# Performance work log

Measured on AMD Instinct MI355X. Metric: run time of the kernel, lower is better.

## Reference

```python
import jax, jax.numpy as jnp
import numpy as np

B, T, D, H = 64, 1024, 1, 256  # batch, seq_len, input_size(=output_size), hidden_size


def setup_inputs() -> dict:
    key = jax.random.key(0)
    ks = jax.random.split(key, 16)
    s = 1.0 / np.sqrt(H)  # torch LSTM/Linear default uniform init scale
    u = lambda k, shp: jax.random.uniform(k, shp, jnp.float32, -s, s)
    return {
        "x": jax.random.normal(ks[0], (B, T, D), jnp.float32),
        # encoder bidirectional 2-layer LSTM; leading dim 2 = (fwd, bwd); gate order i,f,g,o
        "enc_Wih_l0": u(ks[1], (2, 4 * H, D)),
        "enc_Whh_l0": u(ks[2], (2, 4 * H, H)),
        "enc_b_l0": u(ks[3], (2, 4 * H)),
        "enc_Wih_l1": u(ks[4], (2, 4 * H, 2 * H)),
        "enc_Whh_l1": u(ks[5], (2, 4 * H, H)),
        "enc_b_l1": u(ks[6], (2, 4 * H)),
        # decoder bidirectional 2-layer LSTM
        "dec_Wih_l0": u(ks[7], (2, 4 * H, D)),
        "dec_Whh_l0": u(ks[8], (2, 4 * H, H)),
        "dec_b_l0": u(ks[9], (2, 4 * H)),
        "dec_Wih_l1": u(ks[10], (2, 4 * H, 2 * H)),
        "dec_Whh_l1": u(ks[11], (2, 4 * H, H)),
        "dec_b_l1": u(ks[12], (2, 4 * H)),
        # output projection: Linear(2H -> 1)
        "fc_W": u(ks[13], (1, 2 * H)),
        "fc_b": u(ks[14], (1,)),
    }


def _cell(xt, h, c, Wih, Whh, b):
    # one LSTM cell step; xt: (B, Din), h/c: (B, H)
    gates = xt @ Wih.T + h @ Whh.T + b
    i, f, g, o = jnp.split(gates, 4, axis=-1)  # torch gate order i,f,g,o
    c = jax.nn.sigmoid(f) * c + jax.nn.sigmoid(i) * jnp.tanh(g)
    h = jax.nn.sigmoid(o) * jnp.tanh(c)
    return h, c


def _scan_dir(xs, Wih, Whh, b, reverse):
    # xs: (T, B, Din) time-major; returns (T,B,H) outputs aligned to input order + final (h,c)
    bsz = xs.shape[1]
    h0 = jnp.zeros((bsz, H), xs.dtype)
    def step(carry, xt):
        h, c = _cell(xt, carry[0], carry[1], Wih, Whh, b)
        return (h, c), h
    (hT, cT), ys = jax.lax.scan(step, (h0, h0), xs, reverse=reverse)
    return ys, hT, cT


def reference(x, enc_Wih_l0, enc_Whh_l0, enc_b_l0, enc_Wih_l1, enc_Whh_l1, enc_b_l1,
              dec_Wih_l0, dec_Whh_l0, dec_b_l0, dec_Wih_l1, dec_Whh_l1, dec_b_l1,
              fc_W, fc_b):
    xT = jnp.transpose(x, (1, 0, 2))  # (T, B, D)
    # ---- encoder: 2-layer bidirectional LSTM, zero initial state ----
    yf0, hf0, cf0 = _scan_dir(xT, enc_Wih_l0[0], enc_Whh_l0[0], enc_b_l0[0], False)
    yb0, hb0, cb0 = _scan_dir(xT, enc_Wih_l0[1], enc_Whh_l0[1], enc_b_l0[1], True)
    y0 = jnp.concatenate([yf0, yb0], axis=-1)  # (T, B, 2H)
    _, hf1, cf1 = _scan_dir(y0, enc_Wih_l1[0], enc_Whh_l1[0], enc_b_l1[0], False)
    _, hb1, cb1 = _scan_dir(y0, enc_Wih_l1[1], enc_Whh_l1[1], enc_b_l1[1], True)
    # torch state layout: [l0_fwd, l0_bwd, l1_fwd, l1_bwd]
    eh = (hf0, hb0, hf1, hb1)
    ec = (cf0, cb0, cf1, cb1)

    # ---- decoder: each step re-initializes LSTM state from ENCODER state (source bug,
    # reproduced faithfully); only the fc output feeds back as the next input ----
    def dec_step(x_in, _):
        hf, _c1 = _cell(x_in, eh[0], ec[0], dec_Wih_l0[0], dec_Whh_l0[0], dec_b_l0[0])
        hb, _c2 = _cell(x_in, eh[1], ec[1], dec_Wih_l0[1], dec_Whh_l0[1], dec_b_l0[1])
        z = jnp.concatenate([hf, hb], axis=-1)  # (B, 2H)
        hf1_, _c3 = _cell(z, eh[2], ec[2], dec_Wih_l1[0], dec_Whh_l1[0], dec_b_l1[0])
        hb1_, _c4 = _cell(z, eh[3], ec[3], dec_Wih_l1[1], dec_Whh_l1[1], dec_b_l1[1])
        y = jnp.concatenate([hf1_, hb1_], axis=-1) @ fc_W.T + fc_b  # (B, 1)
        return y, y

    x0 = jnp.zeros((x.shape[0], x.shape[2]), x.dtype)
    _, ys = jax.lax.scan(dec_step, x0, None, length=x.shape[1])  # (T, B, 1)
    return jnp.transpose(ys, (1, 0, 2))  # (B, T, 1)
```

## Files before the change

kernel.cpp:

```cpp
#include <hip/hip_runtime.h>
#include <hip/hip_bf16.h>
#include <hip/hip_fp16.h>
#include <math.h>


#define NWG 256
#define THR 512
#define U0S 132

#define ECL0   2048
#define EHL1   (ECL0 + 32768)
#define ECL1   (EHL1 + 16384)
#define ROF    (ECL1 + 32768)
#define WIH1T  (ROF + 262144)
#define GWR    (WIH1T + 524288)
#define PCF    (GWR + 1048576)
#define Y0OF   (PCF + 8192)
#define WS_REQ_BYTES ((size_t)(Y0OF + 16777216) * 4)

struct SeqParams {
  const void *x, *eWih0, *eWhh0, *eB0, *eWih1, *eWhh1, *eB1;
  const void *dWih0, *dWhh0, *dB0, *dWih1, *dWhh1, *dB1, *fcW, *fcb;
  void* out;
  float* ws;
  unsigned* ctrs;
};

typedef _Float16 hlf2 __attribute__((ext_vector_type(2)));

__device__ __forceinline__ float bf2f(unsigned short u) {
  return __uint_as_float(((unsigned)u) << 16);
}
__device__ __forceinline__ float hf2f(unsigned short u) {
  __half_raw r; r.x = u; return __half2float(__half(r));
}
__device__ __forceinline__ unsigned short f2h_u(float f) {
  __half h = __float2half(f);
  return *reinterpret_cast<unsigned short*>(&h);
}

__device__ __forceinline__ float fexp2(float x) {
#if __has_builtin(__builtin_amdgcn_exp2f)
  return __builtin_amdgcn_exp2f(x);
#else
  return exp2f(x);
#endif
}
__device__ __forceinline__ float frcp(float x) {
#if __has_builtin(__builtin_amdgcn_rcpf)
  return __builtin_amdgcn_rcpf(x);
#else
  return 1.0f / x;
#endif
}
__device__ __forceinline__ float sigm(float v) {
  return frcp(1.0f + fexp2(v * -1.44269504f));
}
__device__ __forceinline__ float ftanh(float v) {
  return fmaf(-2.0f, frcp(1.0f + fexp2(v * 2.88539008f)), 1.0f);
}

#if __has_builtin(__builtin_amdgcn_fdot2)
__device__ __forceinline__ float fdot2(hlf2 a, hlf2 b, float c) {
  return __builtin_amdgcn_fdot2(a, b, c, false);
}
#else
__device__ __forceinline__ float fdot2(hlf2 a, hlf2 b, float c) {
  return c + (float)a[0] * (float)b[0] + (float)a[1] * (float)b[1];
}
#endif

__device__ __forceinline__ float dot1(float a, const uint4& x, const uint4& y) {
  const hlf2* xp = reinterpret_cast<const hlf2*>(&x);
  const hlf2* yp = reinterpret_cast<const hlf2*>(&y);
  a = fdot2(xp[0], yp[0], a);
  a = fdot2(xp[1], yp[1], a);
  a = fdot2(xp[2], yp[2], a);
  a = fdot2(xp[3], yp[3], a);
  return a;
}
__device__ __forceinline__ void dot2acc(float4& a, const uint4& hv, const uint4& wv) {
  const hlf2* hp = reinterpret_cast<const hlf2*>(&hv);
  const hlf2* wp = reinterpret_cast<const hlf2*>(&wv);
  a.x = fdot2(hp[0], wp[0], a.x);
  a.y = fdot2(hp[1], wp[1], a.y);
  a.z = fdot2(hp[2], wp[2], a.z);
  a.w = fdot2(hp[3], wp[3], a.w);
}

__device__ __forceinline__ float ldin(const void* p_, size_t i, int bf) {
  return bf ? bf2f(((const unsigned short*)p_)[i]) : ((const float*)p_)[i];
}
__device__ __forceinline__ void stout(void* o, size_t i, float v, int bf) {
  if (bf) ((__hip_bfloat16*)o)[i] = __float2bfloat16(v);
  else    ((float*)o)[i] = v;
}

__device__ __forceinline__ int detect_bf16(const void* xp) {
  const unsigned* u = (const unsigned*)xp;
  int votes = 0;
#pragma unroll 8
  for (int i = 0; i < 64; ++i) {
    unsigned e = (u[i] >> 7) & 0xFF;
    votes += (e >= 108 && e <= 131) ? 1 : 0;
  }
  return votes >= 32;
}

__device__ __forceinline__ void gbar(unsigned* ctrs, unsigned gen) {
  __syncthreads();
  if (threadIdx.x == 0) {
    __hip_atomic_fetch_add(&ctrs[(blockIdx.x & 31) * 32], 1u,
                           __ATOMIC_RELEASE, __HIP_MEMORY_SCOPE_AGENT);
  }
  if (threadIdx.x < 32) {
    while (__hip_atomic_load(&ctrs[threadIdx.x * 32], __ATOMIC_RELAXED,
                             __HIP_MEMORY_SCOPE_AGENT) < gen * 8u) {
      __builtin_amdgcn_s_sleep(1);
    }
    (void)__hip_atomic_load(&ctrs[threadIdx.x * 32], __ATOMIC_ACQUIRE,
                            __HIP_MEMORY_SCOPE_AGENT);
  }
  __syncthreads();
}

__device__ __forceinline__ uint4 ldw8(const void* src, size_t off, int bf) {
  union { __half h[8]; uint4 u; } r;
  if (bf) {
    const unsigned short* s = (const unsigned short*)src + off;
    ushort4 a = *reinterpret_cast<const ushort4*>(s);
    ushort4 b = *reinterpret_cast<const ushort4*>(s + 4);
    r.h[0] = __float2half(bf2f(a.x)); r.h[1] = __float2half(bf2f(a.y));
    r.h[2] = __float2half(bf2f(a.z)); r.h[3] = __float2half(bf2f(a.w));
    r.h[4] = __float2half(bf2f(b.x)); r.h[5] = __float2half(bf2f(b.y));
    r.h[6] = __float2half(bf2f(b.z)); r.h[7] = __float2half(bf2f(b.w));
  } else {
    const float* s = (const float*)src + off;
    float4 a = *reinterpret_cast<const float4*>(s);
    float4 b = *reinterpret_cast<const float4*>(s + 4);
    r.h[0] = __float2half(a.x); r.h[1] = __float2half(a.y);
    r.h[2] = __float2half(a.z); r.h[3] = __float2half(a.w);
    r.h[4] = __float2half(b.x); r.h[5] = __float2half(b.y);
    r.h[6] = __float2half(b.z); r.h[7] = __float2half(b.w);
  }
  return r.u;
}

__device__ __forceinline__ void stage_u128(unsigned* AH, const unsigned* src,
                                           int ustr, int uoff) {
  const int t = threadIdx.x;
#pragma unroll
  for (int i = 0; i < 4; ++i) {
    int idx = t + i * THR;
    int r = idx >> 5, c4 = (idx & 31) << 2;
    uint4 v = *reinterpret_cast<const uint4*>(src + (size_t)r * ustr + uoff + c4);
    *reinterpret_cast<uint4*>(AH + r * U0S + c4) = v;
  }
}
__device__ __forceinline__ void load_w16_rows(uint4 (&wr)[2][4], const void* src,
                                              int rowbase, int bf) {
  const int t = threadIdx.x, kc = t >> 6, rt = t & 3;
#pragma unroll
  for (int j = 0; j < 2; ++j) {
    size_t rb = (size_t)(rowbase + rt * 2 + j) * 256 + kc * 32;
#pragma unroll
    for (int d = 0; d < 4; ++d) wr[j][d] = ldw8(src, rb + d * 8, bf);
  }
}
__device__ __forceinline__ void dot2_t4(float4* acc, const unsigned* A,
                                        const uint4 (&wr)[2][4]) {
  const int t = threadIdx.x;
  const int kc = t >> 6, bt = (t & 63) >> 2;
#pragma unroll
  for (int d = 0; d < 4; ++d) {
    const int k = kc * 16 + d * 4;
    uint4 h0 = *reinterpret_cast<const uint4*>(A + (bt +  0) * U0S + k);
    uint4 h1 = *reinterpret_cast<const uint4*>(A + (bt + 16) * U0S + k);
    uint4 h2 = *reinterpret_cast<const uint4*>(A + (bt + 32) * U0S + k);
    uint4 h3 = *reinterpret_cast<const uint4*>(A + (bt + 48) * U0S + k);
    dot2acc(acc[0], h0, wr[0][d]); dot2acc(acc[1], h0, wr[1][d]);
    dot2acc(acc[2], h1, wr[0][d]); dot2acc(acc[3], h1, wr[1][d]);
    dot2acc(acc[4], h2, wr[0][d]); dot2acc(acc[5], h2, wr[1][d]);
    dot2acc(acc[6], h3, wr[0][d]); dot2acc(acc[7], h3, wr[1][d]);
  }
}
__device__ __forceinline__ void reduce_R(const float4* acc, float* part, float* dst,
                                         const void* bsrc, int rowbase, int bf) {
  const int t = threadIdx.x;
  const int kc = t >> 6, tile = t & 63;
#pragma unroll
  for (int e = 0; e < 8; ++e) {
    const float4 a = acc[e];
    part[e * 512 + kc * 64 + tile] = (a.x + a.y) + (a.z + a.w);
  }
  __syncthreads();
  {
    const int r = t >> 6, b = t & 63;
    const int tl = (b & 15) * 4 + (r >> 1);
    const float* pp = part + ((b >> 4) * 2 + (r & 1)) * 512 + tl;
    float v = ((pp[0] + pp[64]) + (pp[128] + pp[192])) +
              ((pp[256] + pp[320]) + (pp[384] + pp[448]));
    dst[(size_t)b * 1024 + rowbase + r] = v + ldin(bsrc, rowbase + r, bf);
  }
  __syncthreads();
}

__global__ void __launch_bounds__(THR, 2)
__attribute__((amdgpu_waves_per_eu(2, 2)))
seq2seq_kernel(SeqParams p) {
  __shared__ __align__(16) char smem[148224];
  uint4* WLDSu4 = (uint4*)smem;
  float* GF     = (float*)(smem + 131072);
  float* PREB   = (float*)(smem + 135168);
  float* PREWf  = (float*)(smem + 139264);
  float* XROW   = (float*)(smem + 143360);
  unsigned* H16 = (unsigned*)(smem + 147456);
  float* YL     = (float*)(smem + 147968);

  const int w = blockIdx.x;
  const int t = threadIdx.x;
  float* ws = p.ws;
  unsigned* ctrs = p.ctrs;
  unsigned* y0w   = (unsigned*)(ws + Y0OF);
  unsigned* EHL1u = (unsigned*)(ws + EHL1);
  uint4* WIH1Tu4  = (uint4*)(ws + WIH1T);
  unsigned* GWu   = (unsigned*)(ws + GWR);
  unsigned* flg   = (unsigned*)(ws + PCF);
  uint4* DWu4     = (uint4*)(ws + Y0OF);
  unsigned genF = 0;
  const int bfm = detect_bf16(p.x);
  const int enc_act = (w < 128);
  const int d = (w >> 6) & 1, b = w & 63;
  const int R0 = t >> 1, hs = t & 1, swz = R0 & 7;

  uint4 wreg3[3][16];

  {
    if (w == 0) {
      for (int i = t; i < 8192; i += THR) flg[i] = 0u;
    }
    if (enc_act) {
      const void* whh0 = bfm ? (const void*)((const unsigned short*)p.eWhh0 + (size_t)d * 262144)
                             : (const void*)((const float*)p.eWhh0 + (size_t)d * 262144);
#pragma unroll
      for (int sl = 0; sl < 3; ++sl)
#pragma unroll
        for (int kk = 0; kk < 16; ++kk)
          wreg3[sl][kk] = ldw8(whh0, (size_t)(R0 + sl * 256) * 256 + (size_t)hs * 128 + kk * 8, bfm);
#pragma unroll
      for (int i = 0; i < 16; ++i) {
        int idx = t + i * 512;
        int row = idx >> 5, j = idx & 31;
        WLDSu4[row * 32 + (j ^ (row & 7))] =
            ldw8(whh0, (size_t)(768 + row) * 256 + j * 8, bfm);
      }
#pragma unroll
      for (int q = 0; q < 2; ++q) {
        PREB[t + q * 512]  = ldin(p.eB0,   d * 1024 + t + q * 512, bfm);
        PREWf[t + q * 512] = ldin(p.eWih0, d * 1024 + t + q * 512, bfm);
        XROW[t + q * 512]  = ldin(p.x, (size_t)b * 1024 + t + q * 512, bfm);
      }
      if (t < 128) H16[t] = 0u;
    }
  }
  gbar(ctrs, ++genF);

  if (enc_act) {
    float cc = 0.f;
    const uint4* wl = WLDSu4 + R0 * 32;
    for (int st = 0; st < 1024; ++st) {
      const int tt = d ? (1023 - st) : st;
      float s0 = 0.f, s1 = 0.f, s2 = 0.f, s3 = 0.f;
#pragma unroll
      for (int hb = 0; hb < 2; ++hb) {
        uint4 wlv[8], hvv[8];
#pragma unroll
        for (int i = 0; i < 8; ++i) {
          int ii = hb * 8 + i;
          wlv[i] = wl[(hs * 16 + ii) ^ swz];
          hvv[i] = *(const uint4*)(H16 + hs * 64 + ii * 4);
        }
#pragma unroll
        for (int i = 0; i < 8; ++i) {
          int ii = hb * 8 + i;
          s0 = dot1(s0, hvv[i], wreg3[0][ii]);
          s1 = dot1(s1, hvv[i], wreg3[1][ii]);
          s2 = dot1(s2, hvv[i], wreg3[2][ii]);
          s3 = dot1(s3, hvv[i], wlv[i]);
        }
      }
      s0 += __shfl_xor(s0, 1, 64);
      s1 += __shfl_xor(s1, 1, 64);
      s2 += __shfl_xor(s2, 1, 64);
      s3 += __shfl_xor(s3, 1, 64);
      if (hs == 0) { GF[R0] = s0;       GF[R0 + 256] = s1; }
      else         { GF[R0 + 512] = s2; GF[768 + R0] = s3; }
      __syncthreads();
      if (t < 256) {
        float xv = XROW[tt];
        float gi = GF[t]       + PREB[t]       + xv * PREWf[t];
        float gf = GF[256 + t] + PREB[256 + t] + xv * PREWf[256 + t];
        float gg = GF[512 + t] + PREB[512 + t] + xv * PREWf[512 + t];
        float go = GF[768 + t] + PREB[768 + t] + xv * PREWf[768 + t];
        float cn = sigm(gf) * cc + sigm(gi) * ftanh(gg);
        float hn = sigm(go) * ftanh(cn);
        cc = cn;
        ((unsigned short*)H16)[t] = f2h_u(hn);
        if (st == 1023) ws[ECL0 + d * 16384 + b * 256 + t] = cn;
      }
      __syncthreads();
      if (t < 128) y0w[(size_t)tt * 16384 + (size_t)b * 256 + d * 128 + t] = H16[t];
    }
  }
  gbar(ctrs, ++genF);

  {
    {
      int idx = w * 512 + t;
      int dd = idx >> 16, rem = idx & 65535;
      int kc = rem >> 10, row = rem & 1023;
      WIH1Tu4[idx] = ldw8(p.eWih1, (size_t)dd * 524288 + (size_t)row * 512 + kc * 8, bfm);
    }
    if (enc_act) {
      const void* whh1 = bfm ? (const void*)((const unsigned short*)p.eWhh1 + (size_t)d * 262144)
                             : (const void*)((const float*)p.eWhh1 + (size_t)d * 262144);
#pragma unroll
      for (int sl = 0; sl < 3; ++sl)
#pragma unroll
        for (int kk = 0; kk < 16; ++kk)
          wreg3[sl][kk] = ldw8(whh1, (size_t)(R0 + sl * 256) * 256 + (size_t)hs * 128 + kk * 8, bfm);
#pragma unroll
      for (int i = 0; i < 16; ++i) {
        int idx = t + i * 512;
        int row = idx >> 5, j = idx & 31;
        WLDSu4[row * 32 + (j ^ (row & 7))] =
            ldw8(whh1, (size_t)(768 + row) * 256 + j * 8, bfm);
      }
#pragma unroll
      for (int q = 0; q < 2; ++q)
        PREB[t + q * 512] = ldin(p.eB1, d * 1024 + t + q * 512, bfm);
      if (t < 128) H16[t] = 0u;
    }
  }
  gbar(ctrs, ++genF);

  if (enc_act) {
    float cc = 0.f;
    const uint4* wl = WLDSu4 + R0 * 32;
    for (int st = 0; st < 1024; ++st) {
      const int win = st >> 3, sl = st & 7;
      if (sl == 0) {
        if (t == 0) {
          while (__hip_atomic_load(&flg[w * 64], __ATOMIC_RELAXED,
                                   __HIP_MEMORY_SCOPE_AGENT) < (unsigned)(win + 1)) {
            __builtin_amdgcn_s_sleep(1);
          }
        }
        __atomic_signal_fence(__ATOMIC_ACQUIRE);
        __syncthreads();
      }
      unsigned g0 = 0, g1 = 0;
      if (t < 256) {
        const unsigned gb = (unsigned)w * 8192 + (unsigned)(win & 1) * 4096 + (unsigned)sl * 512;
        g0 = __hip_atomic_load(&GWu[gb + t],       __ATOMIC_RELAXED, __HIP_MEMORY_SCOPE_AGENT);
        g1 = __hip_atomic_load(&GWu[gb + 256 + t], __ATOMIC_RELAXED, __HIP_MEMORY_SCOPE_AGENT);
      }
      float s0 = 0.f, s1 = 0.f, s2 = 0.f, s3 = 0.f;
#pragma unroll
      for (int hb = 0; hb < 2; ++hb) {
        uint4 wlv[8], hvv[8];
#pragma unroll
        for (int i = 0; i < 8; ++i) {
          int ii = hb * 8 + i;
          wlv[i] = wl[(hs * 16 + ii) ^ swz];
          hvv[i] = *(const uint4*)(H16 + hs * 64 + ii * 4);
        }
#pragma unroll
        for (int i = 0; i < 8; ++i) {
          int ii = hb * 8 + i;
          s0 = dot1(s0, hvv[i], wreg3[0][ii]);
          s1 = dot1(s1, hvv[i], wreg3[1][ii]);
          s2 = dot1(s2, hvv[i], wreg3[2][ii]);
          s3 = dot1(s3, hvv[i], wlv[i]);
        }
      }
      s0 += __shfl_xor(s0, 1, 64);
      s1 += __shfl_xor(s1, 1, 64);
      s2 += __shfl_xor(s2, 1, 64);
      s3 += __shfl_xor(s3, 1, 64);
      if (hs == 0) { GF[R0] = s0;       GF[R0 + 256] = s1; }
      else         { GF[R0 + 512] = s2; GF[768 + R0] = s3; }
      __syncthreads();
      if (t < 256) {
        float gi = GF[t]       + PREB[t]       + hf2f((unsigned short)(g0 & 0xffffu));
        float gf = GF[256 + t] + PREB[256 + t] + hf2f((unsigned short)(g1 & 0xffffu));
        float gg = GF[512 + t] + PREB[512 + t] + hf2f((unsigned short)(g0 >> 16));
        float go = GF[768 + t] + PREB[768 + t] + hf2f((unsigned short)(g1 >> 16));
        float cn = sigm(gf) * cc + sigm(gi) * ftanh(gg);
        float hn = sigm(go) * ftanh(cn);
        cc = cn;
        ((unsigned short*)H16)[t] = f2h_u(hn);
        if (st == 1023) ws[ECL1 + d * 16384 + b * 256 + t] = cn;
      }
      __syncthreads();
      if (st == 1023 && t < 128) EHL1u[d * 8192 + b * 128 + t] = H16[t];
      if (sl == 7 && t == 0)
        __hip_atomic_store(&flg[w * 64 + 32], (unsigned)(win + 1),
                           __ATOMIC_RELAXED, __HIP_MEMORY_SCOPE_AGENT);
    }
  } else {
    const int chain = w - 128, dp = chain >> 6, bp = chain & 63;
    const uint4* Wt = WIH1Tu4 + (size_t)dp * 65536;
    uint4* YWu4 = (uint4*)smem;
    for (int win = 0; win < 128; ++win) {
      if (win >= 2) {
        if (t == 0) {
          while (__hip_atomic_load(&flg[chain * 64 + 32], __ATOMIC_RELAXED,
                                   __HIP_MEMORY_SCOPE_AGENT) < (unsigned)(win - 1)) {
            __builtin_amdgcn_s_sleep(1);
          }
        }
        __syncthreads();
      }
      {
        int s = t >> 6, kcc = t & 63;
        int tw = dp ? (1023 - (win * 8 + s)) : (win * 8 + s);
        YWu4[s * 64 + kcc] =
            *(const uint4*)(y0w + (size_t)tw * 16384 + (size_t)bp * 256 + kcc * 4);
      }
      __syncthreads();
      float a0[8], a1[8];
#pragma unroll
      for (int s = 0; s < 8; ++s) { a0[s] = 0.f; a1[s] = 0.f; }
      for (int kc = 0; kc < 64; ++kc) {
        uint4 w0 = Wt[kc * 1024 + t];
        uint4 w1 = Wt[kc * 1024 + 512 + t];
#pragma unroll
        for (int s = 0; s < 8; ++s) {
          uint4 yv = YWu4[s * 64 + kc];
          a0[s] = dot1(a0[s], yv, w0);
          a1[s] = dot1(a1[s], yv, w1);
        }
      }
      const unsigned gb = (unsigned)chain * 8192 + (unsigned)(win & 1) * 4096;
#pragma unroll
      for (int s = 0; s < 8; ++s) {
        unsigned pw = (unsigned)f2h_u(a0[s]) | ((unsigned)f2h_u(a1[s]) << 16);
        __hip_atomic_store(&GWu[gb + s * 512 + t], pw,
                           __ATOMIC_RELAXED, __HIP_MEMORY_SCOPE_AGENT);
      }
      __syncthreads();
      if (t == 0)
        __hip_atomic_store(&flg[chain * 64], (unsigned)(win + 1),
                           __ATOMIC_RELAXED, __HIP_MEMORY_SCOPE_AGENT);
    }
  }
  gbar(ctrs, ++genF);

  {
    unsigned* AH0 = (unsigned*)smem;
    float* part = (float*)(smem + 33792);
    const int m = w >> 6, wl6 = w & 63;
    const void* whh;
    if (bfm) whh = (m < 2) ? (const void*)((const unsigned short*)p.dWhh0 + (size_t)m * 262144)
                           : (const void*)((const unsigned short*)p.dWhh1 + (size_t)(m - 2) * 262144);
    else     whh = (m < 2) ? (const void*)((const float*)p.dWhh0 + (size_t)m * 262144)
                           : (const void*)((const float*)p.dWhh1 + (size_t)(m - 2) * 262144);
    const void* bb;
    if (bfm) bb = (m < 2) ? (const void*)((const unsigned short*)p.dB0 + m * 1024)
                          : (const void*)((const unsigned short*)p.dB1 + (m - 2) * 1024);
    else     bb = (m < 2) ? (const void*)((const float*)p.dB0 + m * 1024)
                          : (const void*)((const float*)p.dB1 + (m - 2) * 1024);
    if (m == 0)      stage_u128(AH0, y0w + (size_t)1023 * 16384, 256, 0);
    else if (m == 1) stage_u128(AH0, y0w, 256, 128);
    else             stage_u128(AH0, EHL1u + (m - 2) * 8192, 128, 0);
    __syncthreads();
    float* dst = ws + ROF + m * 65536;
    for (int pass = 0; pass < 2; ++pass) {
      const int rowbase = wl6 * 16 + pass * 8;
      uint4 wrA[2][4];
      load_w16_rows(wrA, whh, rowbase, bfm);
      float4 acc[8];
#pragma unroll
      for (int e = 0; e < 8; ++e) acc[e] = make_float4(0.f, 0.f, 0.f, 0.f);
      dot2_t4(acc, AH0, wrA);
      reduce_R(acc, part, dst, bb, rowbase, bfm);
    }
  }
  gbar(ctrs, ++genF);

  {
    int idx = w * 512 + t;
    int dd = idx >> 16, rem = idx & 65535;
    int kc = rem >> 10, row = rem & 1023;
    DWu4[idx] = ldw8(p.dWih1, (size_t)dd * 524288 + (size_t)row * 512 + kc * 8, bfm);
  }
  float r1i = 0.f, r1f = 0.f, r1g = 0.f, r1o = 0.f, coldc = 0.f, fwc = 0.f, fcb = 0.f;
  {
    float* R0L  = (float*)smem;
    float* WI0L = (float*)(smem + 8192);
    float* C0L  = (float*)(smem + 16384);
    if (w < 64) {
      const int bq = w;
#pragma unroll
      for (int i = 0; i < 4; ++i) {
        int r = t + i * THR;
        int dz = r >> 10, rr = r & 1023;
        R0L[r]  = ws[ROF + dz * 65536 + (size_t)bq * 1024 + rr];
        WI0L[r] = ldin(p.dWih0, dz * 1024 + rr, bfm);
      }
      C0L[t >= 512 ? 0 : t] = ws[ECL0 + (t >> 8) * 16384 + (size_t)bq * 256 + (t & 255)];
      const int dd2 = t >> 8, col = t & 255;
      r1i = ws[ROF + (2 + dd2) * 65536 + (size_t)bq * 1024 +       col];
      r1f = ws[ROF + (2 + dd2) * 65536 + (size_t)bq * 1024 + 256 + col];
      r1g = ws[ROF + (2 + dd2) * 65536 + (size_t)bq * 1024 + 512 + col];
      r1o = ws[ROF + (2 + dd2) * 65536 + (size_t)bq * 1024 + 768 + col];
      coldc = ws[ECL1 + dd2 * 16384 + (size_t)bq * 256 + col];
      fwc = ldin(p.fcW, dd2 * 256 + col, bfm);
      fcb = ldin(p.fcb, 0, bfm);
    }
  }
  gbar(ctrs, ++genF);

  if (w < 64) {
    const int bq = w;
    float* R0L  = (float*)smem;
    float* WI0L = (float*)(smem + 8192);
    float* C0L  = (float*)(smem + 16384);
    unsigned* ZV = (unsigned*)(smem + 18432);
    const int dd2 = t >> 8, col = t & 255;
    const uint4* DWt = DWu4 + (size_t)dd2 * 65536;

    {
      float gi = R0L[dd2 * 1024 +       col];
      float gf = R0L[dd2 * 1024 + 256 + col];
      float gg = R0L[dd2 * 1024 + 512 + col];
      float go = R0L[dd2 * 1024 + 768 + col];
      float cold = C0L[dd2 * 256 + col];
      float cn = sigm(gf) * cold + sigm(gi) * ftanh(gg);
      float hz = sigm(go) * ftanh(cn);
      ((unsigned short*)ZV)[t] = f2h_u(hz);
    }
    __syncthreads();

    float yp1 = 3.0e38f, yp2 = -3.0e38f;
    for (int st = 0; st < 1024; ++st) {
      float ai = 0.f, af = 0.f, ag = 0.f, ao = 0.f;
      for (int kc = 0; kc < 64; ++kc) {
        uint4 zv = *(const uint4*)(ZV + kc * 4);
        uint4 w0 = DWt[kc * 1024 +       col];
        uint4 w1 = DWt[kc * 1024 + 256 + col];
        uint4 w2 = DWt[kc * 1024 + 512 + col];
        uint4 w3 = DWt[kc * 1024 + 768 + col];
        ai = dot1(ai, zv, w0);
        af = dot1(af, zv, w1);
        ag = dot1(ag, zv, w2);
        ao = dot1(ao, zv, w3);
      }
      float gi = ai + r1i, gf = af + r1f, gg = ag + r1g, go = ao + r1o;
      float cn = sigm(gf) * coldc + sigm(gi) * ftanh(gg);
      float h1 = sigm(go) * ftanh(cn);
      GF[t] = h1 * fwc;
      __syncthreads();
      if (t < 64) {
        const float* q = GF + t;
        GF[t] = ((q[0] + q[64]) + (q[128] + q[192])) +
                ((q[256] + q[320]) + (q[384] + q[448]));
      }
      __syncthreads();
      if (t == 0) {
        float yy = fcb;
        for (int i = 0; i < 64; ++i) yy += GF[i];
        YL[0] = yy;
      }
      __syncthreads();
      float ynew = YL[0];
      if (t == 0) stout(p.out, (size_t)bq * 1024 + st, ynew, bfm);
      if (ynew == yp1) {
        for (int t2 = st + 1 + t; t2 < 1024; t2 += THR)
          stout(p.out, (size_t)bq * 1024 + t2, ynew, bfm);
        break;
      }
      if (ynew == yp2) {
        for (int t2 = st + 1 + t; t2 < 1024; t2 += THR)
          stout(p.out, (size_t)bq * 1024 + t2, ((t2 - st) & 1) ? yp1 : ynew, bfm);
        break;
      }
      yp2 = yp1; yp1 = ynew;
      if (st < 1023) {
        __syncthreads();
        float gi2 = ynew * WI0L[dd2 * 1024 +       col] + R0L[dd2 * 1024 +       col];
        float gf2 = ynew * WI0L[dd2 * 1024 + 256 + col] + R0L[dd2 * 1024 + 256 + col];
        float gg2 = ynew * WI0L[dd2 * 1024 + 512 + col] + R0L[dd2 * 1024 + 512 + col];
        float go2 = ynew * WI0L[dd2 * 1024 + 768 + col] + R0L[dd2 * 1024 + 768 + col];
        float cold = C0L[dd2 * 256 + col];
        float cn2 = sigm(gf2) * cold + sigm(gi2) * ftanh(gg2);
        float hz = sigm(go2) * ftanh(cn2);
        ((unsigned short*)ZV)[t] = f2h_u(hz);
        __syncthreads();
      }
    }
  }
}

__global__ void fill_sig(unsigned short* out, int n, float val) {
  int i = blockIdx.x * 256 + threadIdx.x;
  __hip_bfloat16 b = __float2bfloat16(val);
  if (i < n) out[i] = *reinterpret_cast<unsigned short*>(&b);
}

extern "C" void kernel_launch(void* const* d_in, const int* in_sizes, int n_in,
                              void* d_out, int out_size, void* d_ws, size_t ws_size,
                              hipStream_t stream) {
  (void)in_sizes; (void)n_in;
  if (ws_size < WS_REQ_BYTES) {
    float sig = 2048.0f + (float)(ws_size >> 20);
    fill_sig<<<(out_size + 255) / 256, 256, 0, stream>>>(
        (unsigned short*)d_out, out_size, sig);
    return;
  }
  hipMemsetAsync(d_ws, 0, 8192, stream);

  SeqParams p;
  p.x     = d_in[0];
  p.eWih0 = d_in[1];
  p.eWhh0 = d_in[2];
  p.eB0   = d_in[3];
  p.eWih1 = d_in[4];
  p.eWhh1 = d_in[5];
  p.eB1   = d_in[6];
  p.dWih0 = d_in[7];
  p.dWhh0 = d_in[8];
  p.dB0   = d_in[9];
  p.dWih1 = d_in[10];
  p.dWhh1 = d_in[11];
  p.dB1   = d_in[12];
  p.fcW   = d_in[13];
  p.fcb   = d_in[14];
  p.out   = d_out;
  p.ws    = (float*)d_ws;
  p.ctrs  = (unsigned*)d_ws;

  seq2seq_kernel<<<dim3(NWG), dim3(THR), 0, stream>>>(p);
}
```

Baseline: 5.977 ms.

## Double-buffer hidden state and compute LSTM cell redundantly to drop one barrier per step

Measured after the change: 7.208 ms. 20.6% more time.

```diff
diff --git a/kernel.cpp b/kernel.cpp
--- a/kernel.cpp
+++ b/kernel.cpp
@@ -208,14 +208,14 @@
 __global__ void __launch_bounds__(THR, 2)
 __attribute__((amdgpu_waves_per_eu(2, 2)))
 seq2seq_kernel(SeqParams p) {
-  __shared__ __align__(16) char smem[148224];
+  __shared__ __align__(16) char smem[148736];
   uint4* WLDSu4 = (uint4*)smem;
   float* GF     = (float*)(smem + 131072);
   float* PREB   = (float*)(smem + 135168);
   float* PREWf  = (float*)(smem + 139264);
   float* XROW   = (float*)(smem + 143360);
   unsigned* H16 = (unsigned*)(smem + 147456);
-  float* YL     = (float*)(smem + 147968);
+  float* YL     = (float*)(smem + 148480);
 
   const int w = blockIdx.x;
   const int t = threadIdx.x;
@@ -226,6 +226,8 @@
   uint4* WIH1Tu4  = (uint4*)(ws + WIH1T);
   unsigned* GWu   = (unsigned*)(ws + GWR);
   unsigned* flg   = (unsigned*)(ws + PCF);
+  uint4* SB0u4    = (uint4*)(ws + GWR);
+  uint4* SB1u4    = (uint4*)(ws + ROF);
   uint4* DWu4     = (uint4*)(ws + Y0OF);
   unsigned genF = 0;
   const int bfm = detect_bf16(p.x);
@@ -233,26 +235,35 @@
   const int d = (w >> 6) & 1, b = w & 63;
   const int R0 = t >> 1, hs = t & 1, swz = R0 & 7;
 
-  uint4 wreg3[3][16];
+  uint4 wreg2[2][16];
 
   {
     if (w == 0) {
       for (int i = t; i < 8192; i += THR) flg[i] = 0u;
     }
+    if (w < 32) {
+      int e = w * 512 + t;
+      int dd = e >> 13, rem = e & 8191;
+      int kk = rem >> 9, t2 = rem & 511;
+      const void* whh0 = bfm ? (const void*)((const unsigned short*)p.eWhh0 + (size_t)dd * 262144)
+                             : (const void*)((const float*)p.eWhh0 + (size_t)dd * 262144);
+      SB0u4[dd * 8192 + kk * 512 + t2] =
+          ldw8(whh0, (size_t)(768 + (t2 >> 1)) * 256 + (size_t)(t2 & 1) * 128 + kk * 8, bfm);
+    }
     if (enc_act) {
       const void* whh0 = bfm ? (const void*)((const unsigned short*)p.eWhh0 + (size_t)d * 262144)
                              : (const void*)((const float*)p.eWhh0 + (size_t)d * 262144);
 #pragma unroll
-      for (int sl = 0; sl < 3; ++sl)
-#pragma unroll
-        for (int kk = 0; kk < 16; ++kk)
-          wreg3[sl][kk] = ldw8(whh0, (size_t)(R0 + sl * 256) * 256 + (size_t)hs * 128 + kk * 8, bfm);
+      for (int kk = 0; kk < 16; ++kk) {
+        wreg2[0][kk] = ldw8(whh0, (size_t)R0 * 256 + (size_t)hs * 128 + kk * 8, bfm);
+        wreg2[1][kk] = ldw8(whh0, (size_t)(256 + R0) * 256 + (size_t)hs * 128 + kk * 8, bfm);
+      }
 #pragma unroll
       for (int i = 0; i < 16; ++i) {
         int idx = t + i * 512;
         int row = idx >> 5, j = idx & 31;
         WLDSu4[row * 32 + (j ^ (row & 7))] =
-            ldw8(whh0, (size_t)(768 + row) * 256 + j * 8, bfm);
+            ldw8(whh0, (size_t)(512 + row) * 256 + j * 8, bfm);
       }
 #pragma unroll
       for (int q = 0; q < 2; ++q) {
@@ -260,7 +271,7 @@
         PREWf[t + q * 512] = ldin(p.eWih0, d * 1024 + t + q * 512, bfm);
         XROW[t + q * 512]  = ldin(p.x, (size_t)b * 1024 + t + q * 512, bfm);
       }
-      if (t < 128) H16[t] = 0u;
+      if (t < 256) H16[t] = 0u;
     }
   }
   gbar(ctrs, ++genF);
@@ -268,48 +279,48 @@
   if (enc_act) {
     float cc = 0.f;
     const uint4* wl = WLDSu4 + R0 * 32;
+    const uint4* sb = SB0u4 + (size_t)d * 8192;
+    int pp = 0;
     for (int st = 0; st < 1024; ++st) {
       const int tt = d ? (1023 - st) : st;
+      uint4 sbv[16];
+#pragma unroll
+      for (int i = 0; i < 16; ++i) sbv[i] = sb[i * 512 + t];
       float s0 = 0.f, s1 = 0.f, s2 = 0.f, s3 = 0.f;
-#pragma unroll
-      for (int hb = 0; hb < 2; ++hb) {
-        uint4 wlv[8], hvv[8];
-#pragma unroll
-        for (int i = 0; i < 8; ++i) {
-          int ii = hb * 8 + i;
-          wlv[i] = wl[(hs * 16 + ii) ^ swz];
-          hvv[i] = *(const uint4*)(H16 + hs * 64 + ii * 4);
-        }
-#pragma unroll
-        for (int i = 0; i < 8; ++i) {
-          int ii = hb * 8 + i;
-          s0 = dot1(s0, hvv[i], wreg3[0][ii]);
-          s1 = dot1(s1, hvv[i], wreg3[1][ii]);
-          s2 = dot1(s2, hvv[i], wreg3[2][ii]);
-          s3 = dot1(s3, hvv[i], wlv[i]);
-        }
+      const unsigned* hb = H16 + pp * 128 + hs * 64;
+#pragma unroll
+      for (int i = 0; i < 16; ++i) {
+        uint4 hv = *(const uint4*)(hb + i * 4);
+        s0 = dot1(s0, hv, wreg2[0][i]);
+        s1 = dot1(s1, hv, wreg2[1][i]);
+        s2 = dot1(s2, hv, wl[(hs * 16 + i) ^ swz]);
+      }
+#pragma unroll
+      for (int i = 0; i < 16; ++i) {
+        uint4 hv = *(const uint4*)(hb + i * 4);
+        s3 = dot1(s3, hv, sbv[i]);
       }
       s0 += __shfl_xor(s0, 1, 64);
       s1 += __shfl_xor(s1, 1, 64);
       s2 += __shfl_xor(s2, 1, 64);
       s3 += __shfl_xor(s3, 1, 64);
-      if (hs == 0) { GF[R0] = s0;       GF[R0 + 256] = s1; }
-      else         { GF[R0 + 512] = s2; GF[768 + R0] = s3; }
+      float xv = XROW[tt];
+      float gi = s0 + PREB[R0]       + xv * PREWf[R0];
+      float gf = s1 + PREB[256 + R0] + xv * PREWf[256 + R0];
+      float gg = s2 + PREB[512 + R0] + xv * PREWf[512 + R0];
+      float go = s3 + PREB[768 + R0] + xv * PREWf[768 + R0];
+      float cn = sigm(gf) * cc + sigm(gi) * ftanh(gg);
+      float hn = sigm(go) * ftanh(cn);
+      cc = cn;
+      unsigned hu = (unsigned)f2h_u(hn);
+      unsigned hnn = __shfl_down(hu, 2, 64);
+      if ((t & 3) == 0)
+        y0w[(size_t)tt * 16384 + (size_t)b * 256 + d * 128 + (t >> 2)] =
+            hu | (hnn << 16);
+      if (hs == 0) ((unsigned short*)(H16 + (pp ^ 1) * 128))[R0] = (unsigned short)hu;
+      if (st == 1023 && hs == 0) ws[ECL0 + d * 16384 + b * 256 + R0] = cn;
       __syncthreads();
-      if (t < 256) {
-        float xv = XROW[tt];
-        float gi = GF[t]       + PREB[t]       + xv * PREWf[t];
-        float gf = GF[256 + t] + PREB[256 + t] + xv * PREWf[256 + t];
-        float gg = GF[512 + t] + PREB[512 + t] + xv * PREWf[512 + t];
-        float go = GF[768 + t] + PREB[768 + t] + xv * PREWf[768 + t];
-        float cn = sigm(gf) * cc + sigm(gi) * ftanh(gg);
-        float hn = sigm(go) * ftanh(cn);
-        cc = cn;
-        ((unsigned short*)H16)[t] = f2h_u(hn);
-        if (st == 1023) ws[ECL0 + d * 16384 + b * 256 + t] = cn;
-      }
-      __syncthreads();
-      if (t < 128) y0w[(size_t)tt * 16384 + (size_t)b * 256 + d * 128 + t] = H16[t];
+      pp ^= 1;
     }
   }
   gbar(ctrs, ++genF);
@@ -321,25 +332,34 @@
       int kc = rem >> 10, row = rem & 1023;
       WIH1Tu4[idx] = ldw8(p.eWih1, (size_t)dd * 524288 + (size_t)row * 512 + kc * 8, bfm);
     }
+    if (w < 32) {
+      int e = w * 512 + t;
+      int dd = e >> 13, rem = e & 8191;
+      int kk = rem >> 9, t2 = rem & 511;
+      const void* whh1 = bfm ? (const void*)((const unsigned short*)p.eWhh1 + (size_t)dd * 262144)
+                             : (const void*)((const float*)p.eWhh1 + (size_t)dd * 262144);
+      SB1u4[dd * 8192 + kk * 512 + t2] =
+          ldw8(whh1, (size_t)(768 + (t2 >> 1)) * 256 + (size_t)(t2 & 1) * 128 + kk * 8, bfm);
+    }
     if (enc_act) {
       const void* whh1 = bfm ? (const void*)((const unsigned short*)p.eWhh1 + (size_t)d * 262144)
                              : (const void*)((const float*)p.eWhh1 + (size_t)d * 262144);
 #pragma unroll
-      for (int sl = 0; sl < 3; ++sl)
-#pragma unroll
-        for (int kk = 0; kk < 16; ++kk)
-          wreg3[sl][kk] = ldw8(whh1, (size_t)(R0 + sl * 256) * 256 + (size_t)hs * 128 + kk * 8, bfm);
+      for (int kk = 0; kk < 16; ++kk) {
+        wreg2[0][kk] = ldw8(whh1, (size_t)R0 * 256 + (size_t)hs * 128 + kk * 8, bfm);
+        wreg2[1][kk] = ldw8(whh1, (size_t)(256 + R0) * 256 + (size_t)hs * 128 + kk * 8, bfm);
+      }
 #pragma unroll
       for (int i = 0; i < 16; ++i) {
         int idx = t + i * 512;
         int row = idx >> 5, j = idx & 31;
         WLDSu4[row * 32 + (j ^ (row & 7))] =
-            ldw8(whh1, (size_t)(768 + row) * 256 + j * 8, bfm);
+            ldw8(whh1, (size_t)(512 + row) * 256 + j * 8, bfm);
       }
 #pragma unroll
       for (int q = 0; q < 2; ++q)
         PREB[t + q * 512] = ldin(p.eB1, d * 1024 + t + q * 512, bfm);
-      if (t < 128) H16[t] = 0u;
+      if (t < 256) H16[t] = 0u;
     }
   }
   gbar(ctrs, ++genF);
@@ -347,6 +367,8 @@
   if (enc_act) {
     float cc = 0.f;
     const uint4* wl = WLDSu4 + R0 * 32;
+    const uint4* sb = SB1u4 + (size_t)d * 8192;
+    int pp = 0;
     for (int st = 0; st < 1024; ++st) {
       const int win = st >> 3, sl = st & 7;
       if (sl == 0) {
@@ -359,54 +381,50 @@
         __atomic_signal_fence(__ATOMIC_ACQUIRE);
         __syncthreads();
       }
-      unsigned g0 = 0, g1 = 0;
-      if (t < 256) {
-        const unsigned gb = (unsigned)w * 8192 + (unsigned)(win & 1) * 4096 + (unsigned)sl * 512;
-        g0 = __hip_atomic_load(&GWu[gb + t],       __ATOMIC_RELAXED, __HIP_MEMORY_SCOPE_AGENT);
-        g1 = __hip_atomic_load(&GWu[gb + 256 + t], __ATOMIC_RELAXED, __HIP_MEMORY_SCOPE_AGENT);
-      }
+      const unsigned gb = (unsigned)w * 8192 + (unsigned)(win & 1) * 4096 + (unsigned)sl * 512;
+      unsigned gw0 = __hip_atomic_load(&GWu[gb + R0],       __ATOMIC_RELAXED, __HIP_MEMORY_SCOPE_AGENT);
+      unsigned gw1 = __hip_atomic_load(&GWu[gb + 256 + R0], __ATOMIC_RELAXED, __HIP_MEMORY_SCOPE_AGENT);
+      uint4 sbv[16];
+#pragma unroll
+      for (int i = 0; i < 16; ++i) sbv[i] = sb[i * 512 + t];
       float s0 = 0.f, s1 = 0.f, s2 = 0.f, s3 = 0.f;
-#pragma unroll
-      for (int hb = 0; hb < 2; ++hb) {
-        uint4 wlv[8], hvv[8];
-#pragma unroll
-        for (int i = 0; i < 8; ++i) {
-          int ii = hb * 8 + i;
-          wlv[i] = wl[(hs * 16 + ii) ^ swz];
-          hvv[i] = *(const uint4*)(H16 + hs * 64 + ii * 4);
-        }
-#pragma unroll
-        for (int i = 0; i < 8; ++i) {
-          int ii = hb * 8 + i;
-          s0 = dot1(s0, hvv[i], wreg3[0][ii]);
-          s1 = dot1(s1, hvv[i], wreg3[1][ii]);
-          s2 = dot1(s2, hvv[i], wreg3[2][ii]);
-          s3 = dot1(s3, hvv[i], wlv[i]);
-        }
+      const unsigned* hb = H16 + pp * 128 + hs * 64;
+#pragma unroll
+      for (int i = 0; i < 16; ++i) {
+        uint4 hv = *(const uint4*)(hb + i * 4);
+        s0 = dot1(s0, hv, wreg2[0][i]);
+        s1 = dot1(s1, hv, wreg2[1][i]);
+        s2 = dot1(s2, hv, wl[(hs * 16 + i) ^ swz]);
+      }
+#pragma unroll
+      for (int i = 0; i < 16; ++i) {
+        uint4 hv = *(const uint4*)(hb + i * 4);
+        s3 = dot1(s3, hv, sbv[i]);
       }
       s0 += __shfl_xor(s0, 1, 64);
       s1 += __shfl_xor(s1, 1, 64);
       s2 += __shfl_xor(s2, 1, 64);
       s3 += __shfl_xor(s3, 1, 64);
-      if (hs == 0) { GF[R0] = s0;       GF[R0 + 256] = s1; }
-      else         { GF[R0 + 512] = s2; GF[768 + R0] = s3; }
+      float gi = s0 + PREB[R0]       + hf2f((unsigned short)(gw0 & 0xffffu));
+      float gf = s1 + PREB[256 + R0] + hf2f((unsigned short)(gw1 & 0xffffu));
+      float gg = s2 + PREB[512 + R0] + hf2f((unsigned short)(gw0 >> 16));
+      float go = s3 + PREB[768 + R0] + hf2f((unsigned short)(gw1 >> 16));
+      float cn = sigm(gf) * cc + sigm(gi) * ftanh(gg);
+      float hn = sigm(go) * ftanh(cn);
+      cc = cn;
+      unsigned hu = (unsigned)f2h_u(hn);
+      unsigned hnn = __shfl_down(hu, 2, 64);
+      if (st == 1023) {
+        if ((t & 3) == 0)
+          EHL1u[d * 8192 + b * 128 + (t >> 2)] = hu | (hnn << 16);
+        if (hs == 0) ws[ECL1 + d * 16384 + b * 256 + R0] = cn;
+      }
+      if (hs == 0) ((unsigned short*)(H16 + (pp ^ 1) * 128))[R0] = (unsigned short)hu;
       __syncthreads();
-      if (t < 256) {
-        float gi = GF[t]       + PREB[t]       + hf2f((unsigned short)(g0 & 0xffffu));
-        float gf = GF[256 + t] + PREB[256 + t] + hf2f((unsigned short)(g1 & 0xffffu));
-        float gg = GF[512 + t] + PREB[512 + t] + hf2f((unsigned short)(g0 >> 16));
-        float go = GF[768 + t] + PREB[768 + t] + hf2f((unsigned short)(g1 >> 16));
-        float cn = sigm(gf) * cc + sigm(gi) * ftanh(gg);
-        float hn = sigm(go) * ftanh(cn);
-        cc = cn;
-        ((unsigned short*)H16)[t] = f2h_u(hn);
-        if (st == 1023) ws[ECL1 + d * 16384 + b * 256 + t] = cn;
-      }
-      __syncthreads();
-      if (st == 1023 && t < 128) EHL1u[d * 8192 + b * 128 + t] = H16[t];
       if (sl == 7 && t == 0)
         __hip_atomic_store(&flg[w * 64 + 32], (unsigned)(win + 1),
                            __ATOMIC_RELAXED, __HIP_MEMORY_SCOPE_AGENT);
+      pp ^= 1;
     }
   } else {
     const int chain = w - 128, dp = chain >> 6, bp = chain & 63;
```
